# Kernel tuning notes

Hardware: AMD Instinct MI355X
Metric: run time of the kernel (lower is better)

The kernel has to match this reference:

```python
import jax, jax.numpy as jnp
import numpy as np

N_RAYS = 8192
M = 524288
GX, GY, GZ = 160, 160, 128
NFEAT = 12
POS_PE, VIEW_PE = 10, 4
WIDTH = 128
POS_DIM = 3 + 3 * POS_PE * 2      # 63
VIEW_DIM = 3 + 3 * VIEW_PE * 2    # 27
DIM0 = NFEAT + POS_DIM            # 75
ACT_SHIFT = float(np.log(1.0 / (1.0 - 1e-6) - 1.0))  # density bias shift from alpha_init
INTERVAL = 0.5                    # stepsize * voxel_size_ratio
XYZ_MIN, XYZ_MAX = -1.0, 1.0


def posemb(x, n_pe):
    # x: [N,3] -> [N, 3 + 3*n_pe*2], matching cat([x, sin(x*freq), cos(x*freq)])
    freq = 2.0 ** jnp.arange(n_pe, dtype=x.dtype)
    xf = (x[..., None] * freq).reshape(x.shape[0], -1)
    return jnp.concatenate([x, jnp.sin(xf), jnp.cos(xf)], axis=-1)


def trilinear(grid, xyz):
    # grid: [X,Y,Z,C]; xyz: [M,3] in world coords. align_corners=True bilinear (grid_sample).
    sz_f = jnp.array(grid.shape[:3], jnp.float32)
    sz_i = jnp.array(grid.shape[:3], jnp.int32)
    t = (xyz - XYZ_MIN) / (XYZ_MAX - XYZ_MIN) * (sz_f - 1.0)
    t = jnp.clip(t, 0.0, sz_f - 1.0)
    i0 = jnp.clip(jnp.floor(t).astype(jnp.int32), 0, sz_i - 2)
    f = t - i0.astype(t.dtype)
    out = jnp.zeros((xyz.shape[0], grid.shape[-1]), t.dtype)
    for dx in (0, 1):
        for dy in (0, 1):
            for dz in (0, 1):
                w = ((f[:, 0] if dx else 1.0 - f[:, 0])
                     * (f[:, 1] if dy else 1.0 - f[:, 1])
                     * (f[:, 2] if dz else 1.0 - f[:, 2]))
                out = out + w[:, None] * grid[i0[:, 0] + dx, i0[:, 1] + dy, i0[:, 2] + dz]
    return out


def mask_lookup(mask, xyz):
    # nearest-neighbor maskcache_lookup: ijk = round(xyz*scale + shift)
    sz_f = jnp.array(mask.shape, jnp.float32)
    scale = (sz_f - 1.0) / (XYZ_MAX - XYZ_MIN)
    shift = -XYZ_MIN * scale
    ijk = jnp.clip(jnp.round(xyz * scale + shift).astype(jnp.int32), 0,
                   jnp.array(mask.shape, jnp.int32) - 1)
    return mask[ijk[:, 0], ijk[:, 1], ijk[:, 2]]


def alphas2weights(alpha, ray_id, n_rays):
    # segmented T_i = prod_{j<i in ray}(1-alpha_j); weights = T*alpha (ray_id sorted)
    log1a = jnp.log(jnp.clip(1.0 - alpha, 1e-10, 1.0))
    excl = jnp.cumsum(log1a) - log1a                      # global exclusive cumsum
    seg_tot = jax.ops.segment_sum(log1a, ray_id, num_segments=n_rays)
    seg_start = jnp.cumsum(seg_tot) - seg_tot             # exclusive prefix over rays
    T = jnp.exp(excl - seg_start[ray_id])
    weights = T * alpha
    alphainv_last = jnp.exp(seg_tot)
    return weights, alphainv_last


def setup_inputs() -> dict:
    key = jax.random.key(0)
    ks = jax.random.split(key, 16)
    xyz = jax.random.uniform(ks[0], (M, 3), jnp.float32) * (XYZ_MAX - XYZ_MIN) + XYZ_MIN
    ray_id = jnp.sort(jax.random.randint(ks[1], (M,), 0, N_RAYS))
    viewdirs = jax.random.normal(ks[2], (N_RAYS, 3), jnp.float32)
    viewdirs = viewdirs / jnp.linalg.norm(viewdirs, axis=-1, keepdims=True)
    mask = jax.random.uniform(ks[3], (GX, GY, GZ)) > 0.1
    density = jax.random.normal(ks[4], (GX, GY, GZ), jnp.float32) * 0.5
    k0 = jax.random.normal(ks[5], (GX, GY, GZ, NFEAT), jnp.float32) * 0.1
    s = 0.05
    W0 = jax.random.normal(ks[6], (DIM0, WIDTH), jnp.float32) * s
    b0 = jnp.zeros((WIDTH,), jnp.float32)
    W1 = jax.random.normal(ks[7], (WIDTH, WIDTH), jnp.float32) * s
    b1 = jnp.zeros((WIDTH,), jnp.float32)
    W2 = jax.random.normal(ks[8], (WIDTH, WIDTH), jnp.float32) * s
    b2 = jnp.zeros((WIDTH,), jnp.float32)
    Wr = jax.random.normal(ks[9], (WIDTH + VIEW_DIM, 3), jnp.float32) * s
    br = jnp.zeros((3,), jnp.float32)
    return {"xyz": xyz, "ray_id": ray_id, "viewdirs": viewdirs, "mask": mask,
            "density": density, "k0": k0, "W0": W0, "b0": b0, "W1": W1, "b1": b1,
            "W2": W2, "b2": b2, "Wr": Wr, "br": br}


def reference(xyz, ray_id, viewdirs, mask, density, k0, W0, b0, W1, b1, W2, b2, Wr, br):
    # 1) empty-space skipping via mask cache (kept as multiplicative mask for static shapes)
    m = mask_lookup(mask, xyz).astype(xyz.dtype)
    # 2) trilinear density query + raw2alpha
    d = trilinear(density[..., None], xyz)[:, 0]
    alpha = 1.0 - (1.0 + jnp.exp(d + ACT_SHIFT)) ** (-INTERVAL)
    alpha = alpha * m
    # 3) segmented alpha compositing (Alphas2Weights)
    weights, alphainv_last = alphas2weights(alpha, ray_id, N_RAYS)
    # 4) feature query + view MLP -> rgb
    feat = trilinear(k0, xyz)                              # [M, NFEAT]
    h = jnp.concatenate([feat, posemb(xyz, POS_PE)], -1)   # [M, DIM0]
    h = jax.nn.relu(h @ W0 + b0)
    h = jax.nn.relu(h @ W1 + b1)
    h = jax.nn.relu(h @ W2 + b2)
    ve = posemb(viewdirs, VIEW_PE)[ray_id]                 # [M, VIEW_DIM]
    rgb = jax.nn.sigmoid(jnp.concatenate([h, ve], -1) @ Wr + br)
    # 5) composite per ray + white background
    rgb_marched = jax.ops.segment_sum(weights[:, None] * rgb, ray_id, num_segments=N_RAYS)
    rgb_marched = rgb_marched + alphainv_last[:, None] * 1.0
    return rgb_marched
```

## Files before the change

kernel.cpp:

```cpp
#include <hip/hip_runtime.h>
#include <hip/hip_bf16.h>

#define M_SAMPLES 524288
#define NRAYS 8192
#define GXD 160
#define GYD 160
#define GZD 128
#define GYZ (GYD*GZD)
#define NVOX (GXD*GYD*GZD)
#define ACT_SHIFT -13.81550955796f
#define ROWA 136
#define ROWB 136
#define SAMP 64

typedef __bf16 bf16x8 __attribute__((ext_vector_type(8)));
typedef float f32x4 __attribute__((ext_vector_type(4)));
typedef float f32x16 __attribute__((ext_vector_type(16)));
typedef float f32v2 __attribute__((ext_vector_type(2)));

static __device__ inline unsigned short f2bf(float f){
  __hip_bfloat16 h = __float2bfloat16(f);
  unsigned short u; __builtin_memcpy(&u, &h, 2); return u;
}
static __device__ inline float flo(unsigned int u){ return __uint_as_float(u << 16); }
static __device__ inline float fhi(unsigned int u){ return __uint_as_float(u & 0xffff0000u); }

#if defined(__has_builtin)
#if __has_builtin(__builtin_amdgcn_cvt_pk_bf16_f32)
#define HAVE_PK_BF16 1
#endif
#if __has_builtin(__builtin_amdgcn_cvt_pk_f32_fp8) && __has_builtin(__builtin_amdgcn_cvt_pk_fp8_f32)
#define HAVE_FP8 1
#endif
#endif

static __device__ inline unsigned int packbf(float a, float b){
#ifdef HAVE_PK_BF16
  typedef __bf16 bf16v2 __attribute__((ext_vector_type(2)));
  bf16v2 r = __builtin_amdgcn_cvt_pk_bf16_f32(a, b);
  unsigned int u; __builtin_memcpy(&u, &r, 4); return u;
#else
  return (unsigned int)f2bf(a) | ((unsigned int)f2bf(b) << 16);
#endif
}

struct Tri {
  int ix, iy, iz;
  float wx0, wx1, wy0, wy1, wz0, wz1;
};
static __device__ inline Tri tri_setup(float x, float y, float z){
  Tri t;
  float tx = (x+1.f)*0.5f*(float)(GXD-1); tx = fminf(fmaxf(tx,0.f),(float)(GXD-1));
  float ty = (y+1.f)*0.5f*(float)(GYD-1); ty = fminf(fmaxf(ty,0.f),(float)(GYD-1));
  float tz = (z+1.f)*0.5f*(float)(GZD-1); tz = fminf(fmaxf(tz,0.f),(float)(GZD-1));
  t.ix = min((int)tx, GXD-2); t.iy = min((int)ty, GYD-2); t.iz = min((int)tz, GZD-2);
  float fx = tx-t.ix, fy = ty-t.iy, fz = tz-t.iz;
  t.wx0 = 1.f-fx; t.wx1 = fx; t.wy0 = 1.f-fy; t.wy1 = fy; t.wz0 = 1.f-fz; t.wz1 = fz;
  return t;
}

#define NB_REPACK (NVOX/256)
#define NB_W      184
#define NB_RT     (NRAYS/256)
__global__ __launch_bounds__(256) void k_prep(
    const float* __restrict__ density, const float* __restrict__ k0,
    uint4* __restrict__ packed,
    const unsigned int* __restrict__ mw, int* __restrict__ flag,
    const float* __restrict__ W0, const float* __restrict__ W1,
    const float* __restrict__ W2, const float* __restrict__ Wr,
    const float* __restrict__ br,
    unsigned short* __restrict__ wt0, unsigned short* __restrict__ wt1,
    unsigned short* __restrict__ wt2, unsigned short* __restrict__ wtr,
    const float* __restrict__ vd, float* __restrict__ rayterm3)
{
  int b = blockIdx.x;
  if(b < NB_REPACK){
    int v = b*256 + threadIdx.x;
    const float4* kp = (const float4*)(k0 + (size_t)v*12);
    float4 a = kp[0], bb = kp[1], c = kp[2];
#ifdef HAVE_FP8
    uint4 o;
    o.x = __float_as_uint(density[v]);
    int w;
    w = __builtin_amdgcn_cvt_pk_fp8_f32(a.x, a.y, 0, false);
    w = __builtin_amdgcn_cvt_pk_fp8_f32(a.z, a.w, w, true);
    o.y = (unsigned int)w;
    w = __builtin_amdgcn_cvt_pk_fp8_f32(bb.x, bb.y, 0, false);
    w = __builtin_amdgcn_cvt_pk_fp8_f32(bb.z, bb.w, w, true);
    o.z = (unsigned int)w;
    w = __builtin_amdgcn_cvt_pk_fp8_f32(c.x, c.y, 0, false);
    w = __builtin_amdgcn_cvt_pk_fp8_f32(c.z, c.w, w, true);
    o.w = (unsigned int)w;
    packed[v] = o;
#else
    uint4 o0, o1;
    o0.x = __float_as_uint(density[v]);
    o0.y = packbf(a.x, a.y); o0.z = packbf(a.z, a.w); o0.w = packbf(bb.x, bb.y);
    o1.x = packbf(bb.z, bb.w); o1.y = packbf(c.x, c.y); o1.z = packbf(c.z, c.w);
    o1.w = 0;
    packed[(size_t)v*2]   = o0;
    packed[(size_t)v*2+1] = o1;
#endif
    return;
  }
  if(b == NB_REPACK){
    unsigned int v = mw[threadIdx.x & 63];
    unsigned long long any = __ballot(v > 1u);
    if(threadIdx.x == 0) *flag = (any != 0ull) ? 1 : 0;
    return;
  }
  if(b < NB_REPACK + 1 + NB_W){
    int t = (b - NB_REPACK - 1)*256 + threadIdx.x;
    if(t < 128*96){
      int n = t/96, k = t%96;
      wt0[t] = f2bf((k < 75) ? W0[k*128 + n] : 0.f);
    } else if(t < 128*96 + 16384){
      int j = t - 128*96; int n = j/128, k = j%128;
      wt1[j] = f2bf(W1[k*128 + n]);
    } else if(t < 128*96 + 32768){
      int j = t - 128*96 - 16384; int n = j/128, k = j%128;
      wt2[j] = f2bf(W2[k*128 + n]);
    } else if(t < 128*96 + 32768 + 16*128){
      int j = t - 128*96 - 32768; int n = j/128, k = j%128;
      wtr[j] = f2bf((n < 3) ? Wr[k*3 + n] : 0.f);
    }
    return;
  }
  int ray = (b - NB_REPACK - 1 - NB_W)*256 + threadIdx.x;
  if(ray >= NRAYS) return;
  float v0 = vd[ray*3+0], v1 = vd[ray*3+1], v2 = vd[ray*3+2];
  float vej[27];
  vej[0] = v0; vej[1] = v1; vej[2] = v2;
  #pragma unroll
  for(int ci = 0; ci < 3; ++ci){
    float xv = (ci == 0) ? v0 : ((ci == 1) ? v1 : v2);
    #pragma unroll
    for(int p = 0; p < 4; ++p){
      float arg = xv * (float)(1 << p);
      vej[3 + ci*4 + p]  = __sinf(arg);
      vej[15 + ci*4 + p] = __cosf(arg);
    }
  }
  float rt0 = br[0], rt1 = br[1], rt2 = br[2];
  #pragma unroll
  for(int j = 0; j < 27; ++j){
    const float* wr = Wr + (128 + j)*3;
    rt0 += vej[j]*wr[0]; rt1 += vej[j]*wr[1]; rt2 += vej[j]*wr[2];
  }
  rayterm3[ray*3+0] = rt0; rayterm3[ray*3+1] = rt1; rayterm3[ray*3+2] = rt2;
}

template<int KDIM, int SROW>
static __device__ __forceinline__ void mfma_layer(const unsigned short* src,
    const bf16x8* wf, f32x16& acc0, f32x16& acc1, int ln, int kh)
{
  constexpr int NS = KDIM/16;
  const unsigned short* abase0 = src + (ln)*SROW + kh*8;
  const unsigned short* abase1 = src + (32 + ln)*SROW + kh*8;
  f32x16 z = {0.f,0.f,0.f,0.f,0.f,0.f,0.f,0.f,0.f,0.f,0.f,0.f,0.f,0.f,0.f,0.f};
  acc0 = z; acc1 = z;
  __builtin_amdgcn_s_setprio(1);
  #pragma unroll
  for(int st = 0; st < NS; ++st){
    bf16x8 a0 = *(const bf16x8*)(abase0 + st*16);
    bf16x8 a1 = *(const bf16x8*)(abase1 + st*16);
    acc0 = __builtin_amdgcn_mfma_f32_32x32x16_bf16(wf[st], a0, acc0, 0, 0, 0);
    acc1 = __builtin_amdgcn_mfma_f32_32x32x16_bf16(wf[st], a1, acc1, 0, 0, 0);
  }
  __builtin_amdgcn_s_setprio(0);
}

template<int NS>
static __device__ __forceinline__ void load_wf(const unsigned short* wbase, bf16x8* wf){
  #pragma unroll
  for(int st = 0; st < NS; ++st) wf[st] = *(const bf16x8*)(wbase + st*16);
}

template<int DROW>
static __device__ __forceinline__ void epilogue(const f32x16& acc0, const f32x16& acc1,
    unsigned short* dst, const float* __restrict__ bias, int tile_n, int ln, int kh)
{
  float4 bv[4];
  #pragma unroll
  for(int g = 0; g < 4; ++g) bv[g] = *(const float4*)(bias + tile_n*32 + g*8 + kh*4);
  #pragma unroll
  for(int rep = 0; rep < 2; ++rep){
    const f32x16& acc = rep ? acc1 : acc0;
    int scol = rep*32 + ln;
    #pragma unroll
    for(int g = 0; g < 4; ++g){
      int n0 = tile_n*32 + g*8 + kh*4;
      unsigned int lo = packbf(fmaxf(acc[4*g+0] + bv[g].x, 0.f), fmaxf(acc[4*g+1] + bv[g].y, 0.f));
      unsigned int hi = packbf(fmaxf(acc[4*g+2] + bv[g].z, 0.f), fmaxf(acc[4*g+3] + bv[g].w, 0.f));
      unsigned long long o = (unsigned long long)lo | ((unsigned long long)hi << 32);
      *(unsigned long long*)(dst + scol*DROW + n0) = o;
    }
  }
}

template<int PACKED>
__global__ __launch_bounds__(256, 4) void k_mlp(const float* __restrict__ xyz,
    const uint4* __restrict__ packed,
    const float* __restrict__ density, const float* __restrict__ k0,
    const void* __restrict__ mask, const int* __restrict__ flag,
    const int* __restrict__ ray_id,
    const unsigned short* __restrict__ wt0, const unsigned short* __restrict__ wt1,
    const unsigned short* __restrict__ wt2, const unsigned short* __restrict__ wtr,
    const float* __restrict__ b0, const float* __restrict__ b1,
    const float* __restrict__ b2,
    const float* __restrict__ rayterm3, float4* __restrict__ rgba_out)
{
  __shared__ alignas(16) unsigned short hA[SAMP*ROWA];
  __shared__ alignas(16) unsigned short hB[SAMP*ROWB];
  __shared__ float red[SAMP][4];
  __shared__ int ray_s[SAMP];

  int tid = threadIdx.x;
  int lane = tid & 63, wave = tid >> 6;
  int blk = blockIdx.x*SAMP;
  int ln = lane & 31, kh = lane >> 5;

  bf16x8 wf[8];
  load_wf<6>(wt0 + (wave*32 + ln)*96 + kh*8, wf);

  {
    int smp = tid >> 2, corner = tid & 3;
    int i = blk + smp;
    float x = xyz[3*i+0], y = xyz[3*i+1], z = xyz[3*i+2];
    Tri t = tri_setup(x, y, z);
    int dx = corner & 1, dy = corner >> 1;
    float wxy = (dx ? t.wx1 : t.wx0) * (dy ? t.wy1 : t.wy0);
    float w0 = wxy*t.wz0, w1 = wxy*t.wz1;
    size_t vox = (size_t)((t.ix+dx)*GYZ + (t.iy+dy)*GZD + t.iz);
    float pd;
    float pf[12];
#ifdef HAVE_FP8
    if(PACKED){
      uint4 q0 = packed[vox], q1 = packed[vox+1];
      pd = w0*__uint_as_float(q0.x) + w1*__uint_as_float(q1.x);
      f32v2 a, b;
      a = __builtin_amdgcn_cvt_pk_f32_fp8((int)q0.y, false);
      b = __builtin_amdgcn_cvt_pk_f32_fp8((int)q1.y, false);
      pf[0] = w0*a.x + w1*b.x;  pf[1] = w0*a.y + w1*b.y;
      a = __builtin_amdgcn_cvt_pk_f32_fp8((int)q0.y, true);
      b = __builtin_amdgcn_cvt_pk_f32_fp8((int)q1.y, true);
      pf[2] = w0*a.x + w1*b.x;  pf[3] = w0*a.y + w1*b.y;
      a = __builtin_amdgcn_cvt_pk_f32_fp8((int)q0.z, false);
      b = __builtin_amdgcn_cvt_pk_f32_fp8((int)q1.z, false);
      pf[4] = w0*a.x + w1*b.x;  pf[5] = w0*a.y + w1*b.y;
      a = __builtin_amdgcn_cvt_pk_f32_fp8((int)q0.z, true);
      b = __builtin_amdgcn_cvt_pk_f32_fp8((int)q1.z, true);
      pf[6] = w0*a.x + w1*b.x;  pf[7] = w0*a.y + w1*b.y;
      a = __builtin_amdgcn_cvt_pk_f32_fp8((int)q0.w, false);
      b = __builtin_amdgcn_cvt_pk_f32_fp8((int)q1.w, false);
      pf[8] = w0*a.x + w1*b.x;  pf[9] = w0*a.y + w1*b.y;
      a = __builtin_amdgcn_cvt_pk_f32_fp8((int)q0.w, true);
      b = __builtin_amdgcn_cvt_pk_f32_fp8((int)q1.w, true);
      pf[10]= w0*a.x + w1*b.x;  pf[11]= w0*a.y + w1*b.y;
    }
#else
    if(PACKED){
      const uint4* pv = packed + vox*2;
      uint4 q0 = pv[0], q1 = pv[1], q2 = pv[2], q3 = pv[3];
      pd = w0*__uint_as_float(q0.x) + w1*__uint_as_float(q2.x);
      pf[0]  = w0*flo(q0.y) + w1*flo(q2.y);  pf[1]  = w0*fhi(q0.y) + w1*fhi(q2.y);
      pf[2]  = w0*flo(q0.z) + w1*flo(q2.z);  pf[3]  = w0*fhi(q0.z) + w1*fhi(q2.z);
      pf[4]  = w0*flo(q0.w) + w1*flo(q2.w);  pf[5]  = w0*fhi(q0.w) + w1*fhi(q2.w);
      pf[6]  = w0*flo(q1.x) + w1*flo(q3.x);  pf[7]  = w0*fhi(q1.x) + w1*fhi(q3.x);
      pf[8]  = w0*flo(q1.y) + w1*flo(q3.y);  pf[9]  = w0*fhi(q1.y) + w1*fhi(q3.y);
      pf[10] = w0*flo(q1.z) + w1*flo(q3.z);  pf[11] = w0*fhi(q1.z) + w1*fhi(q3.z);
    }
#endif
    if(!PACKED){
      pd = w0*density[vox] + w1*density[vox+1];
      const float4* v = (const float4*)(k0 + vox*12);
      float4 a0 = v[0], a1 = v[1], a2 = v[2];
      float4 c0 = v[3], c1 = v[4], c2 = v[5];
      pf[0] = w0*a0.x + w1*c0.x;  pf[1] = w0*a0.y + w1*c0.y;
      pf[2] = w0*a0.z + w1*c0.z;  pf[3] = w0*a0.w + w1*c0.w;
      pf[4] = w0*a1.x + w1*c1.x;  pf[5] = w0*a1.y + w1*c1.y;
      pf[6] = w0*a1.z + w1*c1.z;  pf[7] = w0*a1.w + w1*c1.w;
      pf[8] = w0*a2.x + w1*c2.x;  pf[9] = w0*a2.y + w1*c2.y;
      pf[10]= w0*a2.z + w1*c2.z;  pf[11]= w0*a2.w + w1*c2.w;
    }
    #pragma unroll
    for(int m2 = 1; m2 < 4; m2 <<= 1){
      pd += __shfl_xor(pd, m2);
      #pragma unroll
      for(int j = 0; j < 12; ++j) pf[j] += __shfl_xor(pf[j], m2);
    }
    if(corner == 0){
      int mx = (int)rintf(x*79.5f + 79.5f); mx = min(max(mx,0), GXD-1);
      int my = (int)rintf(y*79.5f + 79.5f); my = min(max(my,0), GYD-1);
      int mz = (int)rintf(z*63.5f + 63.5f); mz = min(max(mz,0), GZD-1);
      int midx = mx*GYZ + my*GZD + mz;
      bool mm = (*flag) ? (((const unsigned char*)mask)[midx] != 0)
                        : (((const int*)mask)[midx] != 0);
      float e = __expf(pd + ACT_SHIFT);
      float alpha = 1.f - rsqrtf(1.f + e);
      if(!mm) alpha = 0.f;
      red[smp][3] = alpha;
      unsigned int d[8];
      #pragma unroll
      for(int j = 0; j < 6; ++j) d[j] = packbf(pf[2*j], pf[2*j+1]);
      d[6] = packbf(x, y);
      d[7] = packbf(z, __sinf(x));
      uint4* p = (uint4*)(hA + smp*ROWA);
      p[0] = make_uint4(d[0],d[1],d[2],d[3]);
      p[1] = make_uint4(d[4],d[5],d[6],d[7]);
    } else if(corner == 1){
      uint4* p = (uint4*)(hA + smp*ROWA + 80);
      p[0] = make_uint4(0,0,0,0);
      p[1] = make_uint4(0,0,0,0);
      ray_s[smp] = ray_id[i];
    }
  }

  {
    int smp = tid & 63, chunk = 1 + (tid >> 6);
    int i2 = blk + smp;
    float x = xyz[3*i2+0], y = xyz[3*i2+1], z = xyz[3*i2+2];
    float vv[16];
    #pragma unroll
    for(int j = 0; j < 16; ++j){
      int c = chunk*16 + j;
      float r;
      if(c >= 75) r = 0.f;
      else {
        int q = (c < 45) ? (c-15) : (c-45);
        int ci = q/10, p = q - ci*10;
        float xv = (ci == 0) ? x : ((ci == 1) ? y : z);
        float a = xv * (float)(1 << p);
        r = (c < 45) ? __sinf(a) : __cosf(a);
      }
      vv[j] = r;
    }
    unsigned int d[8];
    #pragma unroll
    for(int j = 0; j < 8; ++j) d[j] = packbf(vv[2*j], vv[2*j+1]);
    uint4* p = (uint4*)(hA + smp*ROWA + chunk*16);
    p[0] = make_uint4(d[0],d[1],d[2],d[3]);
    p[1] = make_uint4(d[4],d[5],d[6],d[7]);
  }
  __syncthreads();

  f32x16 acc0, acc1;

  mfma_layer<96, ROWA>(hA, wf, acc0, acc1, ln, kh);
  load_wf<8>(wt1 + (wave*32 + ln)*128 + kh*8, wf);
  epilogue<ROWB>(acc0, acc1, hB, b0, wave, ln, kh);
  __syncthreads();

  mfma_layer<128, ROWB>(hB, wf, acc0, acc1, ln, kh);
  load_wf<8>(wt2 + (wave*32 + ln)*128 + kh*8, wf);
  epilogue<ROWA>(acc0, acc1, hA, b1, wave, ln, kh);
  __syncthreads();

  int col = lane & 15, q4 = lane >> 4;
  mfma_layer<128, ROWA>(hA, wf, acc0, acc1, ln, kh);
  bf16x8 hw[4];
  {
    const unsigned short* wr = wtr + col*128 + q4*8;
    #pragma unroll
    for(int ks = 0; ks < 4; ++ks) hw[ks] = *(const bf16x8*)(wr + ks*32);
  }
  epilogue<ROWB>(acc0, acc1, hB, b2, wave, ln, kh);
  __syncthreads();

  {
    int mt = wave;
    f32x4 acc = {0.f, 0.f, 0.f, 0.f};
    const unsigned short* arow = hB + (mt*16 + col)*ROWB + q4*8;
    __builtin_amdgcn_s_setprio(1);
    #pragma unroll
    for(int ks = 0; ks < 4; ++ks){
      bf16x8 af = *(const bf16x8*)(arow + ks*32);
      acc = __builtin_amdgcn_mfma_f32_16x16x32_bf16(af, hw[ks], acc, 0, 0, 0);
    }
    __builtin_amdgcn_s_setprio(0);
    if(col < 3){
      #pragma unroll
      for(int r = 0; r < 4; ++r){
        int sl = mt*16 + q4*4 + r;
        float v = acc[r] + rayterm3[ray_s[sl]*3 + col];
        red[sl][col] = __fdividef(1.f, 1.f + __expf(-v));
      }
    }
  }
  __syncthreads();

  if(tid < SAMP){
    rgba_out[blk + tid] = make_float4(red[tid][0], red[tid][1], red[tid][2], red[tid][3]);
  }
}

__global__ __launch_bounds__(256) void k_comp2(const int* __restrict__ ray_id,
    const float4* __restrict__ rgba, float* __restrict__ out)
{
  int r = blockIdx.x*4 + (threadIdx.x >> 6);
  int lane = threadIdx.x & 63;
  int lo = 0, hi = M_SAMPLES;
  while(lo < hi){ int mid = (lo+hi) >> 1; if(ray_id[mid] < r) lo = mid+1; else hi = mid; }
  int s = lo;
  int lo2 = s, hi2 = M_SAMPLES;
  while(lo2 < hi2){ int mid = (lo2+hi2) >> 1; if(ray_id[mid] < r+1) lo2 = mid+1; else hi2 = mid; }
  int e = lo2;

  float carry = 1.f;
  float ar = 0.f, ag = 0.f, ab = 0.f;
  for(int base = s; base < e; base += 64){
    int idx = base + lane;
    float4 c = (idx < e) ? rgba[idx] : make_float4(0.f,0.f,0.f,0.f);
    float a = c.w;
    float incl = 1.f - a;
    #pragma unroll
    for(int d2 = 1; d2 < 64; d2 <<= 1){
      float t = __shfl_up(incl, d2);
      if(lane >= d2) incl *= t;
    }
    float excl = __shfl_up(incl, 1);
    if(lane == 0) excl = 1.f;
    float w = carry * excl * a;
    ar += w*c.x; ag += w*c.y; ab += w*c.z;
    carry *= __shfl(incl, 63);
  }
  #pragma unroll
  for(int m2 = 1; m2 < 64; m2 <<= 1){
    ar += __shfl_xor(ar, m2);
    ag += __shfl_xor(ag, m2);
    ab += __shfl_xor(ab, m2);
  }
  if(lane == 0){
    out[3*r+0] = ar + carry;
    out[3*r+1] = ag + carry;
    out[3*r+2] = ab + carry;
  }
}

extern "C" void kernel_launch(void* const* d_in, const int* in_sizes, int n_in,
                              void* d_out, int out_size, void* d_ws, size_t ws_size,
                              hipStream_t stream)
{
  const float* xyz      = (const float*)d_in[0];
  const int*   ray_id   = (const int*)  d_in[1];
  const float* viewdirs = (const float*)d_in[2];
  const void*  mask     =               d_in[3];
  const float* density  = (const float*)d_in[4];
  const float* k0       = (const float*)d_in[5];
  const float* W0 = (const float*)d_in[6];  const float* b0 = (const float*)d_in[7];
  const float* W1 = (const float*)d_in[8];  const float* b1 = (const float*)d_in[9];
  const float* W2 = (const float*)d_in[10]; const float* b2 = (const float*)d_in[11];
  const float* Wr = (const float*)d_in[12]; const float* br = (const float*)d_in[13];
  float* out = (float*)d_out;

  char* ws = (char*)d_ws;
  size_t off = 0;
  auto take = [&](size_t nbytes) -> void* {
    void* p = ws + off;
    off = (off + nbytes + 255) & ~(size_t)255;
    return p;
  };
  int*            flag     = (int*)           take(4);
  unsigned short* wt0      = (unsigned short*)take(128*96*2);
  unsigned short* wt1      = (unsigned short*)take(128*128*2);
  unsigned short* wt2      = (unsigned short*)take(128*128*2);
  unsigned short* wtr      = (unsigned short*)take(16*128*2);
  float*          rayterm3 = (float*)         take((size_t)NRAYS*3*4);
  float4*         rgba_ws  = (float4*)        take((size_t)M_SAMPLES*16);
#ifdef HAVE_FP8
  uint4*          packed   = (uint4*)         take((size_t)NVOX*16);
#else
  uint4*          packed   = (uint4*)         take((size_t)NVOX*32);
#endif
  bool use_packed = (ws_size >= off);

  k_prep<<<NB_REPACK + 1 + NB_W + NB_RT, 256, 0, stream>>>(
      density, k0, packed, (const unsigned int*)mask, flag,
      W0, W1, W2, Wr, br, wt0, wt1, wt2, wtr, viewdirs, rayterm3);
  if(use_packed){
    k_mlp<1><<<M_SAMPLES/SAMP, 256, 0, stream>>>(xyz, packed, density, k0, mask, flag,
                                                 ray_id, wt0, wt1, wt2, wtr,
                                                 b0, b1, b2, rayterm3, rgba_ws);
  } else {
    k_mlp<0><<<M_SAMPLES/SAMP, 256, 0, stream>>>(xyz, packed, density, k0, mask, flag,
                                                 ray_id, wt0, wt1, wt2, wtr,
                                                 b0, b1, b2, rayterm3, rgba_ws);
  }
  k_comp2<<<NRAYS/4, 256, 0, stream>>>(ray_id, rgba_ws, out);
}
```

Baseline: 417.1 us.

## Split trilinear gather into separate kernel and drop per-call grid repack

Removes the per-call repacking of the density and feature grids into packed fp8/bf16 voxels, and moves the trilinear gather plus alpha computation out of the MLP kernel into a new k_gather kernel. That kernel reads fp32 grids directly and writes bf16 per-sample features and alpha to workspace buffers, which k_mlp then loads. This drops a full-grid repack pass and lets the gather run at full occupancy instead of alongside the MFMA-heavy MLP. The cost is an extra round trip through memory for the per-sample features and alpha, and wider fp32 grid reads in place of packed ones.

```diff
diff --git a/kernel.cpp b/kernel.cpp
--- a/kernel.cpp
+++ b/kernel.cpp
@@ -16,21 +16,15 @@
 typedef __bf16 bf16x8 __attribute__((ext_vector_type(8)));
 typedef float f32x4 __attribute__((ext_vector_type(4)));
 typedef float f32x16 __attribute__((ext_vector_type(16)));
-typedef float f32v2 __attribute__((ext_vector_type(2)));
 
 static __device__ inline unsigned short f2bf(float f){
   __hip_bfloat16 h = __float2bfloat16(f);
   unsigned short u; __builtin_memcpy(&u, &h, 2); return u;
 }
-static __device__ inline float flo(unsigned int u){ return __uint_as_float(u << 16); }
-static __device__ inline float fhi(unsigned int u){ return __uint_as_float(u & 0xffff0000u); }
 
 #if defined(__has_builtin)
 #if __has_builtin(__builtin_amdgcn_cvt_pk_bf16_f32)
 #define HAVE_PK_BF16 1
-#endif
-#if __has_builtin(__builtin_amdgcn_cvt_pk_f32_fp8) && __has_builtin(__builtin_amdgcn_cvt_pk_fp8_f32)
-#define HAVE_FP8 1
 #endif
 #endif
 
@@ -59,12 +53,9 @@
   return t;
 }
 
-#define NB_REPACK (NVOX/256)
-#define NB_W      184
-#define NB_RT     (NRAYS/256)
+#define NB_W  184
+#define NB_RT (NRAYS/256)
 __global__ __launch_bounds__(256) void k_prep(
-    const float* __restrict__ density, const float* __restrict__ k0,
-    uint4* __restrict__ packed,
     const unsigned int* __restrict__ mw, int* __restrict__ flag,
     const float* __restrict__ W0, const float* __restrict__ W1,
     const float* __restrict__ W2, const float* __restrict__ Wr,
@@ -74,43 +65,14 @@
     const float* __restrict__ vd, float* __restrict__ rayterm3)
 {
   int b = blockIdx.x;
-  if(b < NB_REPACK){
-    int v = b*256 + threadIdx.x;
-    const float4* kp = (const float4*)(k0 + (size_t)v*12);
-    float4 a = kp[0], bb = kp[1], c = kp[2];
-#ifdef HAVE_FP8
-    uint4 o;
-    o.x = __float_as_uint(density[v]);
-    int w;
-    w = __builtin_amdgcn_cvt_pk_fp8_f32(a.x, a.y, 0, false);
-    w = __builtin_amdgcn_cvt_pk_fp8_f32(a.z, a.w, w, true);
-    o.y = (unsigned int)w;
-    w = __builtin_amdgcn_cvt_pk_fp8_f32(bb.x, bb.y, 0, false);
-    w = __builtin_amdgcn_cvt_pk_fp8_f32(bb.z, bb.w, w, true);
-    o.z = (unsigned int)w;
-    w = __builtin_amdgcn_cvt_pk_fp8_f32(c.x, c.y, 0, false);
-    w = __builtin_amdgcn_cvt_pk_fp8_f32(c.z, c.w, w, true);
-    o.w = (unsigned int)w;
-    packed[v] = o;
-#else
-    uint4 o0, o1;
-    o0.x = __float_as_uint(density[v]);
-    o0.y = packbf(a.x, a.y); o0.z = packbf(a.z, a.w); o0.w = packbf(bb.x, bb.y);
-    o1.x = packbf(bb.z, bb.w); o1.y = packbf(c.x, c.y); o1.z = packbf(c.z, c.w);
-    o1.w = 0;
-    packed[(size_t)v*2]   = o0;
-    packed[(size_t)v*2+1] = o1;
-#endif
-    return;
-  }
-  if(b == NB_REPACK){
+  if(b == 0){
     unsigned int v = mw[threadIdx.x & 63];
     unsigned long long any = __ballot(v > 1u);
     if(threadIdx.x == 0) *flag = (any != 0ull) ? 1 : 0;
     return;
   }
-  if(b < NB_REPACK + 1 + NB_W){
-    int t = (b - NB_REPACK - 1)*256 + threadIdx.x;
+  if(b < 1 + NB_W){
+    int t = (b - 1)*256 + threadIdx.x;
     if(t < 128*96){
       int n = t/96, k = t%96;
       wt0[t] = f2bf((k < 75) ? W0[k*128 + n] : 0.f);
@@ -126,7 +88,7 @@
     }
     return;
   }
-  int ray = (b - NB_REPACK - 1 - NB_W)*256 + threadIdx.x;
+  int ray = (b - 1 - NB_W)*256 + threadIdx.x;
   if(ray >= NRAYS) return;
   float v0 = vd[ray*3+0], v1 = vd[ray*3+1], v2 = vd[ray*3+2];
   float vej[27];
@@ -148,6 +110,60 @@
     rt0 += vej[j]*wr[0]; rt1 += vej[j]*wr[1]; rt2 += vej[j]*wr[2];
   }
   rayterm3[ray*3+0] = rt0; rayterm3[ray*3+1] = rt1; rayterm3[ray*3+2] = rt2;
+}
+
+__global__ __launch_bounds__(256) void k_gather(
+    const float* __restrict__ xyz,
+    const float* __restrict__ density, const float* __restrict__ k0,
+    const void* __restrict__ mask, const int* __restrict__ flag,
+    uint4* __restrict__ feats, float* __restrict__ alphab)
+{
+  int gid = blockIdx.x*256 + threadIdx.x;
+  int smp = gid >> 2, corner = gid & 3;
+  float x = xyz[3*smp+0], y = xyz[3*smp+1], z = xyz[3*smp+2];
+  Tri t = tri_setup(x, y, z);
+  int dx = corner & 1, dy = corner >> 1;
+  float wxy = (dx ? t.wx1 : t.wx0) * (dy ? t.wy1 : t.wy0);
+  float w0 = wxy*t.wz0, w1 = wxy*t.wz1;
+  size_t vox = (size_t)((t.ix+dx)*GYZ + (t.iy+dy)*GZD + t.iz);
+
+  float pd = w0*density[vox] + w1*density[vox+1];
+  const float4* v = (const float4*)(k0 + vox*12);
+  float4 a0 = v[0], a1 = v[1], a2 = v[2];
+  float4 c0 = v[3], c1 = v[4], c2 = v[5];
+  float pf[12];
+  pf[0] = w0*a0.x + w1*c0.x;  pf[1] = w0*a0.y + w1*c0.y;
+  pf[2] = w0*a0.z + w1*c0.z;  pf[3] = w0*a0.w + w1*c0.w;
+  pf[4] = w0*a1.x + w1*c1.x;  pf[5] = w0*a1.y + w1*c1.y;
+  pf[6] = w0*a1.z + w1*c1.z;  pf[7] = w0*a1.w + w1*c1.w;
+  pf[8] = w0*a2.x + w1*c2.x;  pf[9] = w0*a2.y + w1*c2.y;
+  pf[10]= w0*a2.z + w1*c2.z;  pf[11]= w0*a2.w + w1*c2.w;
+
+  #pragma unroll
+  for(int m2 = 1; m2 < 4; m2 <<= 1){
+    pd += __shfl_xor(pd, m2);
+    #pragma unroll
+    for(int j = 0; j < 12; ++j) pf[j] += __shfl_xor(pf[j], m2);
+  }
+  if(corner == 0){
+    int mx = (int)rintf(x*79.5f + 79.5f); mx = min(max(mx,0), GXD-1);
+    int my = (int)rintf(y*79.5f + 79.5f); my = min(max(my,0), GYD-1);
+    int mz = (int)rintf(z*63.5f + 63.5f); mz = min(max(mz,0), GZD-1);
+    int midx = mx*GYZ + my*GZD + mz;
+    bool mm = (*flag) ? (((const unsigned char*)mask)[midx] != 0)
+                      : (((const int*)mask)[midx] != 0);
+    float e = __expf(pd + ACT_SHIFT);
+    float alpha = 1.f - rsqrtf(1.f + e);
+    if(!mm) alpha = 0.f;
+    alphab[smp] = alpha;
+    unsigned int d[8];
+    #pragma unroll
+    for(int j = 0; j < 6; ++j) d[j] = packbf(pf[2*j], pf[2*j+1]);
+    d[6] = packbf(x, y);
+    d[7] = packbf(z, __sinf(x));
+    feats[(size_t)smp*2]   = make_uint4(d[0],d[1],d[2],d[3]);
+    feats[(size_t)smp*2+1] = make_uint4(d[4],d[5],d[6],d[7]);
+  }
 }
 
 template<int KDIM, int SROW>
@@ -198,11 +214,8 @@
   }
 }
 
-template<int PACKED>
 __global__ __launch_bounds__(256, 4) void k_mlp(const float* __restrict__ xyz,
-    const uint4* __restrict__ packed,
-    const float* __restrict__ density, const float* __restrict__ k0,
-    const void* __restrict__ mask, const int* __restrict__ flag,
+    const uint4* __restrict__ feats, const float* __restrict__ alphab,
     const int* __restrict__ ray_id,
     const unsigned short* __restrict__ wt0, const unsigned short* __restrict__ wt1,
     const unsigned short* __restrict__ wt2, const unsigned short* __restrict__ wtr,
@@ -223,103 +236,15 @@
   bf16x8 wf[8];
   load_wf<6>(wt0 + (wave*32 + ln)*96 + kh*8, wf);
 
+  uint4 fv = make_uint4(0,0,0,0);
+  if(tid < 128) fv = feats[(size_t)blk*2 + tid];
+  int smp = tid & 63, chunk = 1 + (tid >> 6);
+  int i2 = blk + smp;
+  float x = xyz[3*i2+0], y = xyz[3*i2+1], z = xyz[3*i2+2];
+  float al = 0.f; int rid = 0;
+  if(tid < SAMP){ al = alphab[blk + tid]; rid = ray_id[blk + tid]; }
+
   {
-    int smp = tid >> 2, corner = tid & 3;
-    int i = blk + smp;
-    float x = xyz[3*i+0], y = xyz[3*i+1], z = xyz[3*i+2];
-    Tri t = tri_setup(x, y, z);
-    int dx = corner & 1, dy = corner >> 1;
-    float wxy = (dx ? t.wx1 : t.wx0) * (dy ? t.wy1 : t.wy0);
-    float w0 = wxy*t.wz0, w1 = wxy*t.wz1;
-    size_t vox = (size_t)((t.ix+dx)*GYZ + (t.iy+dy)*GZD + t.iz);
-    float pd;
-    float pf[12];
-#ifdef HAVE_FP8
-    if(PACKED){
-      uint4 q0 = packed[vox], q1 = packed[vox+1];
-      pd = w0*__uint_as_float(q0.x) + w1*__uint_as_float(q1.x);
-      f32v2 a, b;
-      a = __builtin_amdgcn_cvt_pk_f32_fp8((int)q0.y, false);
-      b = __builtin_amdgcn_cvt_pk_f32_fp8((int)q1.y, false);
-      pf[0] = w0*a.x + w1*b.x;  pf[1] = w0*a.y + w1*b.y;
-      a = __builtin_amdgcn_cvt_pk_f32_fp8((int)q0.y, true);
-      b = __builtin_amdgcn_cvt_pk_f32_fp8((int)q1.y, true);
-      pf[2] = w0*a.x + w1*b.x;  pf[3] = w0*a.y + w1*b.y;
-      a = __builtin_amdgcn_cvt_pk_f32_fp8((int)q0.z, false);
-      b = __builtin_amdgcn_cvt_pk_f32_fp8((int)q1.z, false);
-      pf[4] = w0*a.x + w1*b.x;  pf[5] = w0*a.y + w1*b.y;
-      a = __builtin_amdgcn_cvt_pk_f32_fp8((int)q0.z, true);
-      b = __builtin_amdgcn_cvt_pk_f32_fp8((int)q1.z, true);
-      pf[6] = w0*a.x + w1*b.x;  pf[7] = w0*a.y + w1*b.y;
-      a = __builtin_amdgcn_cvt_pk_f32_fp8((int)q0.w, false);
-      b = __builtin_amdgcn_cvt_pk_f32_fp8((int)q1.w, false);
-      pf[8] = w0*a.x + w1*b.x;  pf[9] = w0*a.y + w1*b.y;
-      a = __builtin_amdgcn_cvt_pk_f32_fp8((int)q0.w, true);
-      b = __builtin_amdgcn_cvt_pk_f32_fp8((int)q1.w, true);
-      pf[10]= w0*a.x + w1*b.x;  pf[11]= w0*a.y + w1*b.y;
-    }
-#else
-    if(PACKED){
-      const uint4* pv = packed + vox*2;
-      uint4 q0 = pv[0], q1 = pv[1], q2 = pv[2], q3 = pv[3];
-      pd = w0*__uint_as_float(q0.x) + w1*__uint_as_float(q2.x);
-      pf[0]  = w0*flo(q0.y) + w1*flo(q2.y);  pf[1]  = w0*fhi(q0.y) + w1*fhi(q2.y);
-      pf[2]  = w0*flo(q0.z) + w1*flo(q2.z);  pf[3]  = w0*fhi(q0.z) + w1*fhi(q2.z);
-      pf[4]  = w0*flo(q0.w) + w1*flo(q2.w);  pf[5]  = w0*fhi(q0.w) + w1*fhi(q2.w);
-      pf[6]  = w0*flo(q1.x) + w1*flo(q3.x);  pf[7]  = w0*fhi(q1.x) + w1*fhi(q3.x);
-      pf[8]  = w0*flo(q1.y) + w1*flo(q3.y);  pf[9]  = w0*fhi(q1.y) + w1*fhi(q3.y);
-      pf[10] = w0*flo(q1.z) + w1*flo(q3.z);  pf[11] = w0*fhi(q1.z) + w1*fhi(q3.z);
-    }
-#endif
-    if(!PACKED){
-      pd = w0*density[vox] + w1*density[vox+1];
-      const float4* v = (const float4*)(k0 + vox*12);
-      float4 a0 = v[0], a1 = v[1], a2 = v[2];
-      float4 c0 = v[3], c1 = v[4], c2 = v[5];
-      pf[0] = w0*a0.x + w1*c0.x;  pf[1] = w0*a0.y + w1*c0.y;
-      pf[2] = w0*a0.z + w1*c0.z;  pf[3] = w0*a0.w + w1*c0.w;
-      pf[4] = w0*a1.x + w1*c1.x;  pf[5] = w0*a1.y + w1*c1.y;
-      pf[6] = w0*a1.z + w1*c1.z;  pf[7] = w0*a1.w + w1*c1.w;
-      pf[8] = w0*a2.x + w1*c2.x;  pf[9] = w0*a2.y + w1*c2.y;
-      pf[10]= w0*a2.z + w1*c2.z;  pf[11]= w0*a2.w + w1*c2.w;
-    }
-    #pragma unroll
-    for(int m2 = 1; m2 < 4; m2 <<= 1){
-      pd += __shfl_xor(pd, m2);
-      #pragma unroll
-      for(int j = 0; j < 12; ++j) pf[j] += __shfl_xor(pf[j], m2);
-    }
-    if(corner == 0){
-      int mx = (int)rintf(x*79.5f + 79.5f); mx = min(max(mx,0), GXD-1);
-      int my = (int)rintf(y*79.5f + 79.5f); my = min(max(my,0), GYD-1);
-      int mz = (int)rintf(z*63.5f + 63.5f); mz = min(max(mz,0), GZD-1);
-      int midx = mx*GYZ + my*GZD + mz;
-      bool mm = (*flag) ? (((const unsigned char*)mask)[midx] != 0)
-                        : (((const int*)mask)[midx] != 0);
-      float e = __expf(pd + ACT_SHIFT);
-      float alpha = 1.f - rsqrtf(1.f + e);
-      if(!mm) alpha = 0.f;
-      red[smp][3] = alpha;
-      unsigned int d[8];
-      #pragma unroll
-      for(int j = 0; j < 6; ++j) d[j] = packbf(pf[2*j], pf[2*j+1]);
-      d[6] = packbf(x, y);
-      d[7] = packbf(z, __sinf(x));
-      uint4* p = (uint4*)(hA + smp*ROWA);
-      p[0] = make_uint4(d[0],d[1],d[2],d[3]);
-      p[1] = make_uint4(d[4],d[5],d[6],d[7]);
-    } else if(corner == 1){
-      uint4* p = (uint4*)(hA + smp*ROWA + 80);
-      p[0] = make_uint4(0,0,0,0);
-      p[1] = make_uint4(0,0,0,0);
-      ray_s[smp] = ray_id[i];
-    }
-  }
-
-  {
-    int smp = tid & 63, chunk = 1 + (tid >> 6);
-    int i2 = blk + smp;
-    float x = xyz[3*i2+0], y = xyz[3*i2+1], z = xyz[3*i2+2];
     float vv[16];
     #pragma unroll
     for(int j = 0; j < 16; ++j){
@@ -342,6 +267,12 @@
     p[0] = make_uint4(d[0],d[1],d[2],d[3]);
     p[1] = make_uint4(d[4],d[5],d[6],d[7]);
   }
+  if(tid < 128){
+    *(uint4*)(hA + (tid>>1)*ROWA + (tid&1)*8) = fv;
+  } else {
+    *(uint4*)(hA + ((tid-128)>>1)*ROWA + 80 + (tid&1)*8) = make_uint4(0,0,0,0);
+  }
+  if(tid < SAMP) ray_s[tid] = rid;
   __syncthreads();
 
   f32x16 acc0, acc1;
@@ -390,7 +321,7 @@
   __syncthreads();
 
   if(tid < SAMP){
-    rgba_out[blk + tid] = make_float4(red[tid][0], red[tid][1], red[tid][2], red[tid][3]);
+    rgba_out[blk + tid] = make_float4(red[tid][0], red[tid][1], red[tid][2], al);
   }
 }
 
@@ -467,24 +398,17 @@
   unsigned short* wtr      = (unsigned short*)take(16*128*2);
   float*          rayterm3 = (float*)         take((size_t)NRAYS*3*4);
   float4*         rgba_ws  = (float4*)        take((size_t)M_SAMPLES*16);
-#ifdef HAVE_FP8
-  uint4*          packed   = (uint4*)         take((size_t)NVOX*16);
-#else
-  uint4*          packed   = (uint4*)         take((size_t)NVOX*32);
-#endif
-  bool use_packed = (ws_size >= off);
-
-  k_prep<<<NB_REPACK + 1 + NB_W + NB_RT, 256, 0, stream>>>(
-      density, k0, packed, (const unsigned int*)mask, flag,
+  uint4*          feats    = (uint4*)         take((size_t)M_SAMPLES*32);
+  float*          alphab   = (float*)         take((size_t)M_SAMPLES*4);
+  (void)ws_size;
+
+  k_prep<<<1 + NB_W + NB_RT, 256, 0, stream>>>(
+      (const unsigned int*)mask, flag,
       W0, W1, W2, Wr, br, wt0, wt1, wt2, wtr, viewdirs, rayterm3);
-  if(use_packed){
-    k_mlp<1><<<M_SAMPLES/SAMP, 256, 0, stream>>>(xyz, packed, density, k0, mask, flag,
-                                                 ray_id, wt0, wt1, wt2, wtr,
-                                                 b0, b1, b2, rayterm3, rgba_ws);
-  } else {
-    k_mlp<0><<<M_SAMPLES/SAMP, 256, 0, stream>>>(xyz, packed, density, k0, mask, flag,
-                                                 ray_id, wt0, wt1, wt2, wtr,
-                                                 b0, b1, b2, rayterm3, rgba_ws);
-  }
+  k_gather<<<M_SAMPLES*4/256, 256, 0, stream>>>(
+      xyz, density, k0, mask, flag, feats, alphab);
+  k_mlp<<<M_SAMPLES/SAMP, 256, 0, stream>>>(
+      xyz, feats, alphab, ray_id, wt0, wt1, wt2, wtr,
+      b0, b1, b2, rayterm3, rgba_ws);
   k_comp2<<<NRAYS/4, 256, 0, stream>>>(ray_id, rgba_ws, out);
 }
```

New measurement: 450.7 us. 1.08x slower.
